# Kernel optimization log

Measured on AMD Instinct MI355X. Metric: run time of the kernel, lower is better.

The kernel has to match this reference:

```python
import jax, jax.numpy as jnp
import numpy as np

B, T, N, M, P = 1024, 128, 128, 256, 256


def _lstm_step(x, h, c, Wih, Whh, bih, bhh):
    # PyTorch LSTM cell: gates ordered i, f, g, o
    g = x @ Wih.T + bih + h @ Whh.T + bhh
    i, f, gg, o = jnp.split(g, 4, axis=-1)
    c_new = jax.nn.sigmoid(f) * c + jax.nn.sigmoid(i) * jnp.tanh(gg)
    h_new = jax.nn.sigmoid(o) * jnp.tanh(c_new)
    return h_new, c_new


def darnn_forward(enc_data, dec_data, enc_Wih, enc_Whh, enc_bih, enc_bhh,
                  We, Ue, ve, Wd, Ud, vd, wt_w, wt_b,
                  dec_Wih, dec_Whh, dec_bih, dec_bhh, l1_w, l1_b, l2_w, l2_b):
    Bsz, Tlen, n = enc_data.shape
    m = enc_Whh.shape[1]
    p = dec_Whh.shape[1]
    # ---- Encoder with input attention ----
    # U_e(data.permute(0,2,1)): (B, n, T); constant across time steps
    Ue_data = jnp.einsum('btn,st->bns', enc_data, Ue)
    def enc_step(carry, x_t):
        h, c = carry                                   # (B, m) each
        q = jnp.concatenate([h, c], axis=-1)           # (B, 2m)
        wq = q @ We.T                                  # (B, T)
        score = jnp.tanh(wq[:, None, :] + Ue_data) @ ve  # (B, n)
        alpha = jax.nn.softmax(score, axis=-1)
        h, c = _lstm_step(alpha * x_t, h, c, enc_Wih, enc_Whh, enc_bih, enc_bhh)
        return (h, c), h
    h0 = jnp.zeros((Bsz, m), enc_data.dtype)
    (_, _), Hs = jax.lax.scan(enc_step, (h0, h0), jnp.swapaxes(enc_data, 0, 1))
    H = jnp.swapaxes(Hs, 0, 1)                         # (B, T, m)
    # ---- Decoder with temporal attention ----
    UH = jnp.einsum('btm,um->btu', H, Ud)              # (B, T, m); constant
    def attn_ctx(d, s):
        q = jnp.concatenate([d, s], axis=-1)           # (B, 2p)
        wq = q @ Wd.T                                  # (B, m)
        score = jnp.tanh(wq[:, None, :] + UH) @ vd     # (B, T)
        beta = jax.nn.softmax(score, axis=-1)
        return jnp.einsum('bt,btm->bm', beta, H)       # (B, m)
    def dec_step(carry, y):
        d, s = carry
        ctx = attn_ctx(d, s)
        y_tilde = jnp.concatenate([y, ctx], axis=-1) @ wt_w.T + wt_b  # (B, 1)
        d, s = _lstm_step(y_tilde, d, s, dec_Wih, dec_Whh, dec_bih, dec_bhh)
        return (d, s), None
    d0 = jnp.zeros((Bsz, p), enc_data.dtype)
    ys = jnp.swapaxes(dec_data[:, :Tlen - 1, :], 0, 1)  # (T-1, B, 1)
    (d, s), _ = jax.lax.scan(dec_step, (d0, d0), ys)
    ctx = attn_ctx(d, s)
    out = jnp.concatenate([d, ctx], axis=-1)            # (B, p + m)
    out = jax.nn.relu(out @ l1_w.T + l1_b) @ l2_w.T + l2_b
    return out.reshape(-1)


def setup_inputs() -> dict:
    key = jax.random.key(0)
    ks = jax.random.split(key, 22)
    f = lambda k, shape: jax.random.normal(k, shape, jnp.float32) * 0.05
    return {
        'enc_data': jax.random.normal(ks[0], (B, T, N), jnp.float32),
        'dec_data': jax.random.normal(ks[1], (B, T, 1), jnp.float32),
        'enc_Wih': f(ks[2], (4 * M, N)), 'enc_Whh': f(ks[3], (4 * M, M)),
        'enc_bih': f(ks[4], (4 * M,)), 'enc_bhh': f(ks[5], (4 * M,)),
        'We': f(ks[6], (T, 2 * M)), 'Ue': f(ks[7], (T, T)), 've': f(ks[8], (T,)),
        'Wd': f(ks[9], (M, 2 * P)), 'Ud': f(ks[10], (M, M)), 'vd': f(ks[11], (M,)),
        'wt_w': f(ks[12], (1, M + 1)), 'wt_b': f(ks[13], (1,)),
        'dec_Wih': f(ks[14], (4 * P, 1)), 'dec_Whh': f(ks[15], (4 * P, P)),
        'dec_bih': f(ks[16], (4 * P,)), 'dec_bhh': f(ks[17], (4 * P,)),
        'l1_w': f(ks[18], (P, M + P)), 'l1_b': f(ks[19], (P,)),
        'l2_w': f(ks[20], (1, P)), 'l2_b': f(ks[21], (1,)),
    }


def reference(enc_data, dec_data, enc_Wih, enc_Whh, enc_bih, enc_bhh,
              We, Ue, ve, Wd, Ud, vd, wt_w, wt_b,
              dec_Wih, dec_Whh, dec_bih, dec_bhh, l1_w, l1_b, l2_w, l2_b):
    return darnn_forward(enc_data, dec_data, enc_Wih, enc_Whh, enc_bih, enc_bhh,
                         We, Ue, ve, Wd, Ud, vd, wt_w, wt_b,
                         dec_Wih, dec_Whh, dec_bih, dec_bhh, l1_w, l1_b, l2_w, l2_b)
```

## Files before the change

kernel.cpp:

```cpp
#include <hip/hip_runtime.h>

typedef unsigned short ushort_t;
typedef unsigned char u8_t;
typedef unsigned int u32_t;
typedef float f32x2 __attribute__((ext_vector_type(2)));

static constexpr int BATCH = 1024;
static constexpr int TT = 128;
static constexpr int NN = 128;
static constexpr int MM = 256;

__device__ __forceinline__ float bf2f(ushort_t u) {
    union { unsigned int i; float f; } v;
    v.i = ((unsigned int)u) << 16;
    return v.f;
}
__device__ __forceinline__ ushort_t f2bf(float f) {
    union { unsigned int i; float f; } v;
    v.f = f;
    unsigned int i = v.i;
    return (ushort_t)((i + 0x7FFFu + ((i >> 16) & 1u)) >> 16);
}
__device__ __forceinline__ u32_t pk2bf(float lo, float hi) {
    return (u32_t)f2bf(lo) | ((u32_t)f2bf(hi) << 16);
}
__device__ __forceinline__ float dot2bf(u32_t a, u32_t b, float c) {
    float d;
    asm("v_dot2_f32_bf16 %0, %1, %2, %3" : "=v"(d) : "v"(a), "v"(b), "v"(c));
    return d;
}
__device__ __forceinline__ void unp8(const int4 w, float* o) {
    union { unsigned int i; float f; } v;
    v.i = ((unsigned int)w.x) << 16;        o[0] = v.f;
    v.i = ((unsigned int)w.x) & 0xffff0000u; o[1] = v.f;
    v.i = ((unsigned int)w.y) << 16;        o[2] = v.f;
    v.i = ((unsigned int)w.y) & 0xffff0000u; o[3] = v.f;
    v.i = ((unsigned int)w.z) << 16;        o[4] = v.f;
    v.i = ((unsigned int)w.z) & 0xffff0000u; o[5] = v.f;
    v.i = ((unsigned int)w.w) << 16;        o[6] = v.f;
    v.i = ((unsigned int)w.w) & 0xffff0000u; o[7] = v.f;
}
__device__ __forceinline__ void unp4(const int2 w, float* o) {
    union { unsigned int i; float f; } v;
    v.i = ((unsigned int)w.x) << 16;        o[0] = v.f;
    v.i = ((unsigned int)w.x) & 0xffff0000u; o[1] = v.f;
    v.i = ((unsigned int)w.y) << 16;        o[2] = v.f;
    v.i = ((unsigned int)w.y) & 0xffff0000u; o[3] = v.f;
}
__device__ __forceinline__ void unp8f8(const int2 w, float* o) {
    f32x2 a = __builtin_amdgcn_cvt_pk_f32_fp8(w.x, false);
    f32x2 b = __builtin_amdgcn_cvt_pk_f32_fp8(w.x, true);
    f32x2 c = __builtin_amdgcn_cvt_pk_f32_fp8(w.y, false);
    f32x2 d = __builtin_amdgcn_cvt_pk_f32_fp8(w.y, true);
    o[0] = a.x; o[1] = a.y; o[2] = b.x; o[3] = b.y;
    o[4] = c.x; o[5] = c.y; o[6] = d.x; o[7] = d.y;
}
__device__ __forceinline__ float tanh_fast(float x) {
    float e = __expf(2.0f * x);
    return 1.0f - __fdividef(2.0f, e + 1.0f);
}
__device__ __forceinline__ float sig_fast(float x) {
    return __fdividef(1.0f, 1.0f + __expf(-x));
}

template<bool WBF16, bool TRANSW, int CMODE, bool RELU>
__global__ __launch_bounds__(256) void gemm_k(
    const float* __restrict__ A1, int lda1, long sA1z, int K1,
    const float* __restrict__ A2, int lda2, int K2,
    const void* __restrict__ W1v, int ldw1, long sW1z,
    const void* __restrict__ W2v, int ldw2,
    const float* __restrict__ bias1,
    void* __restrict__ Cv, int ldc, long sCz)
{
    __shared__ float As[32][68];
    __shared__ float Ws[32][68];
    const int tid = threadIdx.x;
    const int z = blockIdx.z;
    const int m0 = blockIdx.y * 64;
    const int g0 = blockIdx.x * 64;
    const int tm = tid & 15, tn = tid >> 4;
    float acc[4][4];
#pragma unroll
    for (int i = 0; i < 4; ++i)
#pragma unroll
        for (int j = 0; j < 4; ++j) acc[i][j] = 0.0f;

    for (int phase = 0; phase < 2; ++phase) {
        const float* A = (phase == 0) ? (A1 + (long)z * sA1z) : A2;
        const int lda = (phase == 0) ? lda1 : lda2;
        const int K = (phase == 0) ? K1 : K2;
        const int ldw = (phase == 0) ? ldw1 : ldw2;
        const void* Wv = (phase == 0) ? W1v : W2v;
        const long woff = (phase == 0) ? (long)z * sW1z : 0;
        if (A == nullptr || Wv == nullptr || K <= 0) continue;

        for (int k0 = 0; k0 < K; k0 += 32) {
            const int rem = K - k0;
            {
                const int tr0 = tid >> 3;
                const int tk = (tid & 7) * 4;
#pragma unroll
                for (int pass = 0; pass < 2; ++pass) {
                    const int m = tr0 + pass * 32;
                    const float* p = A + (long)(m0 + m) * lda + k0 + tk;
#pragma unroll
                    for (int j = 0; j < 4; ++j) {
                        float v = 0.0f;
                        if (tk + j < rem) v = p[j];
                        As[tk + j][m] = v;
                    }
                }
            }
            if constexpr (TRANSW) {
                const float* W = (const float*)Wv + woff;
                const int gq = (tid & 15) * 4;
                const int kr = tid >> 4;
#pragma unroll
                for (int pass = 0; pass < 2; ++pass) {
                    const int k = kr + pass * 16;
                    const float* p = W + (long)(k0 + k) * ldw + g0 + gq;
                    const bool ok = (k < rem);
#pragma unroll
                    for (int j = 0; j < 4; ++j) {
                        float v = 0.0f;
                        if (ok) v = p[j];
                        Ws[k][gq + j] = v;
                    }
                }
            } else if constexpr (WBF16) {
                const ushort_t* W = (const ushort_t*)Wv + woff;
                const int g = tid >> 2;
                const int tk = (tid & 3) * 8;
                const ushort_t* p = W + (long)(g0 + g) * ldw + k0 + tk;
#pragma unroll
                for (int j = 0; j < 8; ++j) {
                    float v = 0.0f;
                    if (tk + j < rem) v = bf2f(p[j]);
                    Ws[tk + j][g] = v;
                }
            } else {
                const float* W = (const float*)Wv + woff;
                const int tr0 = tid >> 3;
                const int tk = (tid & 7) * 4;
#pragma unroll
                for (int pass = 0; pass < 2; ++pass) {
                    const int g = tr0 + pass * 32;
                    const float* p = W + (long)(g0 + g) * ldw + k0 + tk;
#pragma unroll
                    for (int j = 0; j < 4; ++j) {
                        float v = 0.0f;
                        if (tk + j < rem) v = p[j];
                        Ws[tk + j][g] = v;
                    }
                }
            }
            __syncthreads();
#pragma unroll
            for (int kk = 0; kk < 32; ++kk) {
                const float4 av = *(const float4*)&As[kk][tm * 4];
                const float4 bv = *(const float4*)&Ws[kk][tn * 4];
                const float a[4] = {av.x, av.y, av.z, av.w};
                const float b[4] = {bv.x, bv.y, bv.z, bv.w};
#pragma unroll
                for (int i = 0; i < 4; ++i)
#pragma unroll
                    for (int j = 0; j < 4; ++j)
                        acc[i][j] = fmaf(a[i], b[j], acc[i][j]);
            }
            __syncthreads();
        }
    }
#pragma unroll
    for (int i = 0; i < 4; ++i) {
        const long m = m0 + tm * 4 + i;
        if constexpr (CMODE == 2) {
            float v[4];
#pragma unroll
            for (int j = 0; j < 4; ++j) {
                v[j] = acc[i][j];
                if (bias1) v[j] += bias1[g0 + tn * 4 + j];
                if (RELU) v[j] = fmaxf(v[j], 0.0f);
            }
            int pk = __builtin_amdgcn_cvt_pk_fp8_f32(v[0], v[1], 0, false);
            pk = __builtin_amdgcn_cvt_pk_fp8_f32(v[2], v[3], pk, true);
            *(unsigned int*)((u8_t*)Cv + (long)z * sCz + m * ldc + g0 + tn * 4) =
                (unsigned int)pk;
        } else {
#pragma unroll
            for (int j = 0; j < 4; ++j) {
                const int g = g0 + tn * 4 + j;
                float v = acc[i][j];
                if (bias1) v += bias1[g];
                if (RELU) v = fmaxf(v, 0.0f);
                if constexpr (CMODE == 1)
                    ((ushort_t*)Cv)[(long)z * sCz + m * ldc + g] = f2bf(v);
                else
                    ((float*)Cv)[(long)z * sCz + m * ldc + g] = v;
            }
        }
    }
}

__global__ void prep_encw_k(const float* __restrict__ Wih, const float* __restrict__ Whh,
                            ushort_t* __restrict__ dst) {
    int i = blockIdx.x * 256 + threadIdx.x;
    if (i >= 384 * 1024) return;
    int k = i >> 10, col = i & 1023, u = col >> 2, q = col & 3, g = q * 256 + u;
    float v = (k < 128) ? Wih[g * 128 + k] : Whh[g * 256 + (k - 128)];
    dst[(k >> 1) * 2048 + u * 8 + q * 2 + (k & 1)] = f2bf(v);
}

__global__ void prep_decw_k(const float* __restrict__ Wih, const float* __restrict__ Whh,
                            ushort_t* __restrict__ dst) {
    int i = blockIdx.x * 256 + threadIdx.x;
    if (i >= 257 * 1024) return;
    int k = i >> 10, col = i & 1023, u = col >> 2, q = col & 3, g = q * 256 + u;
    float v = (k == 0) ? Wih[g] : Whh[g * 256 + (k - 1)];
    ushort_t b = f2bf(v);
    if (k == 0) {
        dst[col] = b;
    } else {
        int kk = k - 1;
        dst[1024 + (kk >> 1) * 2048 + u * 8 + q * 2 + (kk & 1)] = b;
    }
}

__global__ void transpose_k(const float* __restrict__ src, float* __restrict__ dst,
                            int R, int C) {
    int i = blockIdx.x * 256 + threadIdx.x;
    if (i < R * C) { int r = i / C, c = i - r * C; dst[c * R + r] = src[i]; }
}

__global__ void packT_k(const float* __restrict__ src, ushort_t* __restrict__ dst,
                        int R, int C) {
    int i = blockIdx.x * 256 + threadIdx.x;
    if (i >= R * C) return;
    int s = i / C, k = i - s * C;
    dst[(k >> 1) * (2 * R) + (s >> 2) * 8 + (s & 3) * 2 + (k & 1)] = f2bf(src[i]);
}

__global__ __launch_bounds__(512) void enc_persist(
    const float* __restrict__ enc_data,
    const u8_t* __restrict__ D,
    const ushort_t* __restrict__ WeB,
    const float* __restrict__ ve,
    const ushort_t* __restrict__ WencB,
    const float* __restrict__ bih, const float* __restrict__ bhh,
    ushort_t* __restrict__ Hbf)
{
    const int tid = threadIdx.x;
    const int b0 = blockIdx.x * 4;
    __shared__ __align__(16) float cs[256][4];
    __shared__ __align__(16) u32_t qpk[256][4];
    __shared__ __align__(16) u32_t xtp[64][4];
    __shared__ __align__(16) float wqp[16][128][4];
    __shared__ __align__(16) float wqs[128][4];
    __shared__ __align__(16) float scp[8][4][128];
    __shared__ float gp[4][4][256];
    __shared__ float ves[128];

    if (tid < 128) ves[tid] = ve[tid];
    if (tid < 256) {
        const float4 z = make_float4(0.f, 0.f, 0.f, 0.f);
        *(float4*)cs[tid] = z;
    }
    {
        uint4 z4 = {0u, 0u, 0u, 0u};
        for (int i = tid; i < 256; i += 512) *(uint4*)qpk[i] = z4;
    }
    const int u = tid & 255;
    const int ks = tid >> 8;
    const float b_i = bih[u] + bhh[u];
    const float b_f = bih[256 + u] + bhh[256 + u];
    const float b_g = bih[512 + u] + bhh[512 + u];
    const float b_o = bih[768 + u] + bhh[768 + u];
    __syncthreads();

    const int kgq = tid >> 5, sv = tid & 31;
    const ushort_t* wq_w = WeB + (long)(kgq * 16) * 256 + sv * 8;
    const int nv = tid & 15, srow = (tid >> 4) & 3, ssl = tid >> 6;
    const u8_t* Dp0 = D + (long)(b0 + srow) * 16384 + (ssl * 16) * 128 + nv * 8;
    const ushort_t* gw = WencB + u * 8;

    float SVe = 0.0f;
#pragma unroll
    for (int s = 0; s < 16; ++s) SVe += ves[ssl * 16 + s];

    for (int t = 0; t < 128; ++t) {
        {
            float a[4][4];
#pragma unroll
            for (int m = 0; m < 4; ++m)
#pragma unroll
                for (int r = 0; r < 4; ++r) a[m][r] = 0.0f;
#pragma unroll 4
            for (int k2 = 0; k2 < 16; ++k2) {
                const uint4 wv = *(const uint4*)(wq_w + k2 * 256);
                const uint4 qv = *(const uint4*)qpk[kgq * 16 + k2];
                const u32_t wa[4] = {wv.x, wv.y, wv.z, wv.w};
                const u32_t qa[4] = {qv.x, qv.y, qv.z, qv.w};
#pragma unroll
                for (int m = 0; m < 4; ++m)
#pragma unroll
                    for (int r = 0; r < 4; ++r)
                        a[m][r] = dot2bf(wa[m], qa[r], a[m][r]);
            }
#pragma unroll
            for (int m = 0; m < 4; ++m)
                *(float4*)wqp[kgq][sv * 4 + m] = make_float4(a[m][0], a[m][1], a[m][2], a[m][3]);
        }
        __syncthreads();
        if (tid < 128) {
            float4 s = *(const float4*)wqp[0][tid];
#pragma unroll
            for (int g = 1; g < 16; ++g) {
                const float4 p = *(const float4*)wqp[g][tid];
                s.x += p.x; s.y += p.y; s.z += p.z; s.w += p.w;
            }
            *(float4*)wqs[tid] = s;
        }
        __syncthreads();
        {
            float a[8];
#pragma unroll
            for (int j = 0; j < 8; ++j) a[j] = 0.0f;
#pragma unroll 4
            for (int s = 0; s < 16; ++s) {
                const int sg = ssl * 16 + s;
                const float w2 = wqs[sg][srow] * 2.0f;
                const float vv = ves[sg];
                const int2 wv2 = *(const int2*)(Dp0 + s * 128);
                float d[8];
                unp8f8(wv2, d);
#pragma unroll
                for (int j = 0; j < 8; ++j) {
                    const float ex = __expf(fmaf(d[j], 2.0f, w2));
                    a[j] = fmaf(vv, __fdividef(1.0f, ex + 1.0f), a[j]);
                }
            }
            *(float4*)&scp[ssl][srow][nv * 8] =
                make_float4(fmaf(-2.f, a[0], SVe), fmaf(-2.f, a[1], SVe),
                            fmaf(-2.f, a[2], SVe), fmaf(-2.f, a[3], SVe));
            *(float4*)&scp[ssl][srow][nv * 8 + 4] =
                make_float4(fmaf(-2.f, a[4], SVe), fmaf(-2.f, a[5], SVe),
                            fmaf(-2.f, a[6], SVe), fmaf(-2.f, a[7], SVe));
        }
        __syncthreads();
        if (tid < 256) {
            const int w = tid >> 6, lane = tid & 63;
            float s0 = 0.0f, s1 = 0.0f;
#pragma unroll
            for (int g = 0; g < 8; ++g) {
                s0 += scp[g][w][lane];
                s1 += scp[g][w][lane + 64];
            }
            float mx = fmaxf(s0, s1);
            for (int o = 32; o > 0; o >>= 1) mx = fmaxf(mx, __shfl_xor(mx, o, 64));
            const float e0 = __expf(s0 - mx), e1 = __expf(s1 - mx);
            float sm = e0 + e1;
            for (int o = 32; o > 0; o >>= 1) sm += __shfl_xor(sm, o, 64);
            const float inv = __fdividef(1.0f, sm);
            const float* xp = enc_data + ((long)(b0 + w) * 128 + t) * 128;
            const float v0 = e0 * inv * xp[lane];
            const float v1 = e1 * inv * xp[lane + 64];
            const float p0 = __shfl_xor(v0, 1, 64);
            const float p1 = __shfl_xor(v1, 1, 64);
            if ((lane & 1) == 0) {
                xtp[lane >> 1][w] = pk2bf(v0, p0);
                xtp[32 + (lane >> 1)][w] = pk2bf(v1, p1);
            }
        }
        __syncthreads();
        float acc[4][4];
#pragma unroll
        for (int q = 0; q < 4; ++q)
#pragma unroll
            for (int r = 0; r < 4; ++r) acc[q][r] = 0.0f;
        if (ks == 0) {
#pragma unroll 4
            for (int p = 0; p < 64; ++p) {
                const uint4 wv = *(const uint4*)(gw + (long)p * 2048);
                const uint4 xv = *(const uint4*)xtp[p];
                const u32_t wa[4] = {wv.x, wv.y, wv.z, wv.w};
                const u32_t xa[4] = {xv.x, xv.y, xv.z, xv.w};
#pragma unroll
                for (int q = 0; q < 4; ++q)
#pragma unroll
                    for (int r = 0; r < 4; ++r)
                        acc[q][r] = dot2bf(wa[q], xa[r], acc[q][r]);
            }
#pragma unroll 4
            for (int p = 64; p < 96; ++p) {
                const uint4 wv = *(const uint4*)(gw + (long)p * 2048);
                const uint4 xv = *(const uint4*)qpk[p - 64];
                const u32_t wa[4] = {wv.x, wv.y, wv.z, wv.w};
                const u32_t xa[4] = {xv.x, xv.y, xv.z, xv.w};
#pragma unroll
                for (int q = 0; q < 4; ++q)
#pragma unroll
                    for (int r = 0; r < 4; ++r)
                        acc[q][r] = dot2bf(wa[q], xa[r], acc[q][r]);
            }
        } else {
#pragma unroll 4
            for (int p = 96; p < 192; ++p) {
                const uint4 wv = *(const uint4*)(gw + (long)p * 2048);
                const uint4 xv = *(const uint4*)qpk[p - 64];
                const u32_t wa[4] = {wv.x, wv.y, wv.z, wv.w};
                const u32_t xa[4] = {xv.x, xv.y, xv.z, xv.w};
#pragma unroll
                for (int q = 0; q < 4; ++q)
#pragma unroll
                    for (int r = 0; r < 4; ++r)
                        acc[q][r] = dot2bf(wa[q], xa[r], acc[q][r]);
            }
#pragma unroll
            for (int q = 0; q < 4; ++q)
#pragma unroll
                for (int r = 0; r < 4; ++r) gp[q][r][u] = acc[q][r];
        }
        __syncthreads();
        if (ks == 0) {
#pragma unroll
            for (int r = 0; r < 4; ++r) {
                const float iv = sig_fast(acc[0][r] + gp[0][r][u] + b_i);
                const float fv = sig_fast(acc[1][r] + gp[1][r][u] + b_f);
                const float gv = tanh_fast(acc[2][r] + gp[2][r][u] + b_g);
                const float ov = sig_fast(acc[3][r] + gp[3][r][u] + b_o);
                const float cn = fv * cs[u][r] + iv * gv;
                const float hn = ov * tanh_fast(cn);
                cs[u][r] = cn;
                const float hp = __shfl_xor(hn, 1, 64);
                const float cp = __shfl_xor(cn, 1, 64);
                if ((u & 1) == 0) {
                    qpk[u >> 1][r] = pk2bf(hn, hp);
                    qpk[128 + (u >> 1)][r] = pk2bf(cn, cp);
                }
                Hbf[((long)(b0 + r) * 128 + t) * 256 + u] = f2bf(hn);
            }
        }
        __syncthreads();
    }
}

__global__ __launch_bounds__(512) void dec_persist(
    const float* __restrict__ dec_data,
    const u8_t* __restrict__ UH2,
    const ushort_t* __restrict__ Hb,
    const ushort_t* __restrict__ WdB,
    const float* __restrict__ vd,
    const ushort_t* __restrict__ WdecB,
    const float* __restrict__ bih, const float* __restrict__ bhh,
    const float* __restrict__ wt_w, const float* __restrict__ wt_b,
    const float* __restrict__ l1T,
    const float* __restrict__ l1_b,
    const float* __restrict__ l2_w, const float* __restrict__ l2_b,
    float* __restrict__ out)
{
    const int tid = threadIdx.x;
    const int b0 = blockIdx.x * 4;
    __shared__ __align__(16) float ds4[256][4];
    __shared__ __align__(16) float ss4[256][4];
    __shared__ __align__(16) u32_t qpk[256][4];
    __shared__ __align__(16) float wqp[8][256][4];
    __shared__ __align__(16) float wqs[256][4];
    __shared__ __align__(16) float scp[8][4][128];
    __shared__ __align__(16) float beta[128][4];
    __shared__ __align__(16) float ctxp[4][4][256];
    __shared__ __align__(16) float ctx4[256][4];
    __shared__ float gp[4][4][256];
    __shared__ __align__(16) float o14[256][4];
    __shared__ float vds[256];
    __shared__ float wt1s[256];
    __shared__ float l2s[256];
    __shared__ __align__(16) float yts[4];

    const int u = tid & 255;
    const int ks = tid >> 8;
    if (tid < 256) {
        vds[tid] = vd[tid];
        wt1s[tid] = wt_w[1 + tid];
        l2s[tid] = l2_w[tid];
        const float4 z = make_float4(0.f, 0.f, 0.f, 0.f);
        *(float4*)ds4[tid] = z;
        *(float4*)ss4[tid] = z;
    }
    {
        uint4 z4 = {0u, 0u, 0u, 0u};
        for (int i = tid; i < 256; i += 512) *(uint4*)qpk[i] = z4;
    }
    const float b_i = bih[u] + bhh[u];
    const float b_f = bih[256 + u] + bhh[256 + u];
    const float b_g = bih[512 + u] + bhh[512 + u];
    const float b_o = bih[768 + u] + bhh[768 + u];
    __syncthreads();

    const int kgq = tid >> 6, mv = tid & 63;
    const ushort_t* wq_w = WdB + (long)(kgq * 32) * 512 + mv * 8;
    const int tv = tid & 15, srow = (tid >> 4) & 3, usl = tid >> 6;
    const u8_t* up0 = UH2 + ((long)(b0 + srow) * 256 + usl * 32) * 128 + tv * 8;
    const int mv8 = tid & 31, crow = (tid >> 5) & 3, ssl2 = tid >> 7;
    const ushort_t* hp0 = Hb + ((long)(b0 + crow) * 128 + ssl2 * 32) * 256 + mv8 * 8;
    const ushort_t* gwp = WdecB + 1024 + u * 8;

    float SVd = 0.0f;
#pragma unroll
    for (int s = 0; s < 32; ++s) SVd += vds[usl * 32 + s];

    for (int td = 0; td < 128; ++td) {
        {
            float a[4][4];
#pragma unroll
            for (int m = 0; m < 4; ++m)
#pragma unroll
                for (int r = 0; r < 4; ++r) a[m][r] = 0.0f;
#pragma unroll 4
            for (int k2 = 0; k2 < 32; ++k2) {
                const uint4 wv = *(const uint4*)(wq_w + k2 * 512);
                const uint4 qv = *(const uint4*)qpk[kgq * 32 + k2];
                const u32_t wa[4] = {wv.x, wv.y, wv.z, wv.w};
                const u32_t qa[4] = {qv.x, qv.y, qv.z, qv.w};
#pragma unroll
                for (int m = 0; m < 4; ++m)
#pragma unroll
                    for (int r = 0; r < 4; ++r)
                        a[m][r] = dot2bf(wa[m], qa[r], a[m][r]);
            }
#pragma unroll
            for (int m = 0; m < 4; ++m)
                *(float4*)wqp[kgq][mv * 4 + m] = make_float4(a[m][0], a[m][1], a[m][2], a[m][3]);
        }
        __syncthreads();
        if (tid < 256) {
            float4 s = *(const float4*)wqp[0][tid];
#pragma unroll
            for (int g = 1; g < 8; ++g) {
                const float4 p = *(const float4*)wqp[g][tid];
                s.x += p.x; s.y += p.y; s.z += p.z; s.w += p.w;
            }
            *(float4*)wqs[tid] = s;
        }
        __syncthreads();
        {
            float a[8];
#pragma unroll
            for (int j = 0; j < 8; ++j) a[j] = 0.0f;
#pragma unroll 4
            for (int uu = 0; uu < 32; ++uu) {
                const int ug = usl * 32 + uu;
                const float w2 = wqs[ug][srow] * 2.0f;
                const float vv = vds[ug];
                const int2 wv2 = *(const int2*)(up0 + uu * 128);
                float d[8];
                unp8f8(wv2, d);
#pragma unroll
                for (int j = 0; j < 8; ++j) {
                    const float ex = __expf(fmaf(d[j], 2.0f, w2));
                    a[j] = fmaf(vv, __fdividef(1.0f, ex + 1.0f), a[j]);
                }
            }
            *(float4*)&scp[usl][srow][tv * 8] =
                make_float4(fmaf(-2.f, a[0], SVd), fmaf(-2.f, a[1], SVd),
                            fmaf(-2.f, a[2], SVd), fmaf(-2.f, a[3], SVd));
            *(float4*)&scp[usl][srow][tv * 8 + 4] =
                make_float4(fmaf(-2.f, a[4], SVd), fmaf(-2.f, a[5], SVd),
                            fmaf(-2.f, a[6], SVd), fmaf(-2.f, a[7], SVd));
        }
        __syncthreads();
        if (tid < 256) {
            const int w = tid >> 6, lane = tid & 63;
            float s0 = 0.0f, s1 = 0.0f;
#pragma unroll
            for (int g = 0; g < 8; ++g) {
                s0 += scp[g][w][lane];
                s1 += scp[g][w][lane + 64];
            }
            float mx = fmaxf(s0, s1);
            for (int o = 32; o > 0; o >>= 1) mx = fmaxf(mx, __shfl_xor(mx, o, 64));
            const float e0 = __expf(s0 - mx), e1 = __expf(s1 - mx);
            float sm = e0 + e1;
            for (int o = 32; o > 0; o >>= 1) sm += __shfl_xor(sm, o, 64);
            const float inv = __fdividef(1.0f, sm);
            beta[lane][w] = e0 * inv;
            beta[lane + 64][w] = e1 * inv;
        }
        __syncthreads();
        {
            float c[8];
#pragma unroll
            for (int j = 0; j < 8; ++j) c[j] = 0.0f;
#pragma unroll 4
            for (int s = 0; s < 32; ++s) {
                const float bt = beta[ssl2 * 32 + s][crow];
                const int4 wv2 = *(const int4*)(hp0 + s * 256);
                float hv[8];
                unp8(wv2, hv);
#pragma unroll
                for (int j = 0; j < 8; ++j)
                    c[j] = fmaf(bt, hv[j], c[j]);
            }
            *(float4*)&ctxp[ssl2][crow][mv8 * 8]     = make_float4(c[0], c[1], c[2], c[3]);
            *(float4*)&ctxp[ssl2][crow][mv8 * 8 + 4] = make_float4(c[4], c[5], c[6], c[7]);
        }
        __syncthreads();
        if (tid < 256) {
            const int m = tid;
            float cr[4];
#pragma unroll
            for (int r = 0; r < 4; ++r)
                cr[r] = ctxp[0][r][m] + ctxp[1][r][m] + ctxp[2][r][m] + ctxp[3][r][m];
            *(float4*)ctx4[m] = make_float4(cr[0], cr[1], cr[2], cr[3]);
        }
        __syncthreads();
        if (td == 127) break;
        if (tid < 256) {
            const int w = tid >> 6, lane = tid & 63;
            float s = ctx4[lane][w] * wt1s[lane]
                    + ctx4[lane + 64][w] * wt1s[lane + 64]
                    + ctx4[lane + 128][w] * wt1s[lane + 128]
                    + ctx4[lane + 192][w] * wt1s[lane + 192];
            for (int o = 32; o > 0; o >>= 1) s += __shfl_xor(s, o, 64);
            if (lane == 0)
                yts[w] = s + wt_b[0] + wt_w[0] * dec_data[(long)(b0 + w) * 128 + td];
        }
        __syncthreads();
        float acc[4][4];
        if (ks == 0) {
            const int2 yv = *(const int2*)(WdecB + u * 4);
            float wy[4]; unp4(yv, wy);
            const float4 y4 = *(const float4*)yts;
            const float ya[4] = {y4.x, y4.y, y4.z, y4.w};
#pragma unroll
            for (int q = 0; q < 4; ++q)
#pragma unroll
                for (int r = 0; r < 4; ++r) acc[q][r] = wy[q] * ya[r];
#pragma unroll 4
            for (int p = 0; p < 64; ++p) {
                const uint4 wv = *(const uint4*)(gwp + (long)p * 2048);
                const uint4 xv = *(const uint4*)qpk[p];
                const u32_t wa[4] = {wv.x, wv.y, wv.z, wv.w};
                const u32_t xa[4] = {xv.x, xv.y, xv.z, xv.w};
#pragma unroll
                for (int q = 0; q < 4; ++q)
#pragma unroll
                    for (int r = 0; r < 4; ++r)
                        acc[q][r] = dot2bf(wa[q], xa[r], acc[q][r]);
            }
        } else {
#pragma unroll
            for (int q = 0; q < 4; ++q)
#pragma unroll
                for (int r = 0; r < 4; ++r) acc[q][r] = 0.0f;
#pragma unroll 4
            for (int p = 64; p < 128; ++p) {
                const uint4 wv = *(const uint4*)(gwp + (long)p * 2048);
                const uint4 xv = *(const uint4*)qpk[p];
                const u32_t wa[4] = {wv.x, wv.y, wv.z, wv.w};
                const u32_t xa[4] = {xv.x, xv.y, xv.z, xv.w};
#pragma unroll
                for (int q = 0; q < 4; ++q)
#pragma unroll
                    for (int r = 0; r < 4; ++r)
                        acc[q][r] = dot2bf(wa[q], xa[r], acc[q][r]);
            }
#pragma unroll
            for (int q = 0; q < 4; ++q)
#pragma unroll
                for (int r = 0; r < 4; ++r) gp[q][r][u] = acc[q][r];
        }
        __syncthreads();
        if (ks == 0) {
#pragma unroll
            for (int r = 0; r < 4; ++r) {
                const float iv = sig_fast(acc[0][r] + gp[0][r][u] + b_i);
                const float fv = sig_fast(acc[1][r] + gp[1][r][u] + b_f);
                const float gv = tanh_fast(acc[2][r] + gp[2][r][u] + b_g);
                const float ov = sig_fast(acc[3][r] + gp[3][r][u] + b_o);
                const float sn = fv * ss4[u][r] + iv * gv;
                const float dn = ov * tanh_fast(sn);
                ss4[u][r] = sn;
                ds4[u][r] = dn;
                const float dp = __shfl_xor(dn, 1, 64);
                const float sp = __shfl_xor(sn, 1, 64);
                if ((u & 1) == 0) {
                    qpk[u >> 1][r] = pk2bf(dn, dp);
                    qpk[128 + (u >> 1)][r] = pk2bf(sn, sp);
                }
            }
        }
        __syncthreads();
    }
    {
        const float* src = l1T + ks * 256 * 256;
        float a0 = 0, a1 = 0, a2 = 0, a3 = 0;
#pragma unroll 4
        for (int k = 0; k < 256; ++k) {
            const float w = src[k * 256 + u];
            const float4 q = (ks == 0) ? *(const float4*)ds4[k]
                                       : *(const float4*)ctx4[k];
            a0 = fmaf(q.x, w, a0); a1 = fmaf(q.y, w, a1);
            a2 = fmaf(q.z, w, a2); a3 = fmaf(q.w, w, a3);
        }
        if (ks == 1) {
            gp[0][0][u] = a0; gp[0][1][u] = a1; gp[0][2][u] = a2; gp[0][3][u] = a3;
        } else {
            gp[1][0][u] = a0; gp[1][1][u] = a1; gp[1][2][u] = a2; gp[1][3][u] = a3;
        }
    }
    __syncthreads();
    if (tid < 256) {
        const float bb = l1_b[tid];
        *(float4*)o14[tid] = make_float4(
            fmaxf(gp[0][0][tid] + gp[1][0][tid] + bb, 0.f),
            fmaxf(gp[0][1][tid] + gp[1][1][tid] + bb, 0.f),
            fmaxf(gp[0][2][tid] + gp[1][2][tid] + bb, 0.f),
            fmaxf(gp[0][3][tid] + gp[1][3][tid] + bb, 0.f));
    }
    __syncthreads();
    if (tid < 256) {
        const int w = tid >> 6, lane = tid & 63;
        float s = o14[lane][w] * l2s[lane]
                + o14[lane + 64][w] * l2s[lane + 64]
                + o14[lane + 128][w] * l2s[lane + 128]
                + o14[lane + 192][w] * l2s[lane + 192];
        for (int o = 32; o > 0; o >>= 1) s += __shfl_xor(s, o, 64);
        if (lane == 0) out[b0 + w] = s + l2_b[0];
    }
}

extern "C" void kernel_launch(void* const* d_in, const int* in_sizes, int n_in,
                              void* d_out, int out_size, void* d_ws, size_t ws_size,
                              hipStream_t stream)
{
    const float* enc_data = (const float*)d_in[0];
    const float* dec_data = (const float*)d_in[1];
    const float* enc_Wih  = (const float*)d_in[2];
    const float* enc_Whh  = (const float*)d_in[3];
    const float* enc_bih  = (const float*)d_in[4];
    const float* enc_bhh  = (const float*)d_in[5];
    const float* We   = (const float*)d_in[6];
    const float* Ue   = (const float*)d_in[7];
    const float* ve   = (const float*)d_in[8];
    const float* Wd   = (const float*)d_in[9];
    const float* Ud   = (const float*)d_in[10];
    const float* vd   = (const float*)d_in[11];
    const float* wt_w = (const float*)d_in[12];
    const float* wt_b = (const float*)d_in[13];
    const float* dec_Wih = (const float*)d_in[14];
    const float* dec_Whh = (const float*)d_in[15];
    const float* dec_bih = (const float*)d_in[16];
    const float* dec_bhh = (const float*)d_in[17];
    const float* l1_w = (const float*)d_in[18];
    const float* l1_b = (const float*)d_in[19];
    const float* l2_w = (const float*)d_in[20];
    const float* l2_b = (const float*)d_in[21];

    ushort_t* Hbf  = (ushort_t*)d_ws;
    u8_t* Dbf      = (u8_t*)(Hbf + (long)BATCH * TT * MM);
    u8_t* UHbf     = Dbf + (long)BATCH * TT * NN;
    ushort_t* WencB = (ushort_t*)(UHbf + (long)BATCH * MM * TT);
    ushort_t* WdecB = WencB + 384 * 1024;
    ushort_t* WeB   = WdecB + 257 * 1024;
    ushort_t* WdB   = WeB + 512 * 128;
    float* l1T      = (float*)(WdB + 512 * 256);

    prep_encw_k<<<1536, 256, 0, stream>>>(enc_Wih, enc_Whh, WencB);
    prep_decw_k<<<1028, 256, 0, stream>>>(dec_Wih, dec_Whh, WdecB);
    packT_k<<<(128 * 512 + 255) / 256, 256, 0, stream>>>(We, WeB, 128, 512);
    packT_k<<<(256 * 512 + 255) / 256, 256, 0, stream>>>(Wd, WdB, 256, 512);
    transpose_k<<<(256 * 512 + 255) / 256, 256, 0, stream>>>(l1_w, l1T, 256, 512);

    gemm_k<false, true, 2, false><<<dim3(NN / 64, TT / 64, BATCH), 256, 0, stream>>>(
        Ue, TT, 0, TT,
        nullptr, 0, 0,
        enc_data, NN, (long)TT * NN,
        nullptr, 0,
        nullptr,
        Dbf, NN, (long)TT * NN);

    enc_persist<<<256, 512, 0, stream>>>(enc_data, Dbf, WeB, ve, WencB,
                                         enc_bih, enc_bhh, Hbf);

    gemm_k<true, false, 2, false><<<dim3(TT / 64, MM / 64, BATCH), 256, 0, stream>>>(
        Ud, MM, 0, MM,
        nullptr, 0, 0,
        Hbf, MM, (long)TT * MM,
        nullptr, 0,
        nullptr,
        UHbf, TT, (long)MM * TT);

    dec_persist<<<256, 512, 0, stream>>>(dec_data, UHbf, Hbf, WdB, vd, WdecB,
                                         dec_bih, dec_bhh, wt_w, wt_b,
                                         l1T, l1_b, l2_w, l2_b, (float*)d_out);
}
```

Before: 9.415 ms.

## Hoist decoder recurrent matmul earlier, pair sigmoid divides, bf16 beta context dot

Moves the decoder LSTM h/s recurrent gate matmul (which depends only on the previous state) up to run alongside the attention query matmul. This removes one barrier and the serial gate phase after the attention and context stages. The tanh-via-exp attention score loop now shares one reciprocal across two elements, with a clamp added to avoid overflow. The context sum packs beta into bf16 pairs and uses v_dot2 with v_perm to interleave H rows. Beta now loses precision to bf16, and the gp exchange relies on the existing barriers for correctness.

Result: faster. 8.004 ms (-15.0%).

```diff
diff --git a/kernel.cpp b/kernel.cpp
--- a/kernel.cpp
+++ b/kernel.cpp
@@ -27,6 +27,11 @@
 __device__ __forceinline__ float dot2bf(u32_t a, u32_t b, float c) {
     float d;
     asm("v_dot2_f32_bf16 %0, %1, %2, %3" : "=v"(d) : "v"(a), "v"(b), "v"(c));
+    return d;
+}
+__device__ __forceinline__ u32_t permb(u32_t s0, u32_t s1, u32_t sel) {
+    u32_t d;
+    asm("v_perm_b32 %0, %1, %2, %3" : "=v"(d) : "v"(s0), "v"(s1), "v"(sel));
     return d;
 }
 __device__ __forceinline__ void unp8(const int4 w, float* o) {
@@ -333,9 +338,13 @@
                 float d[8];
                 unp8f8(wv2, d);
 #pragma unroll
-                for (int j = 0; j < 8; ++j) {
-                    const float ex = __expf(fmaf(d[j], 2.0f, w2));
-                    a[j] = fmaf(vv, __fdividef(1.0f, ex + 1.0f), a[j]);
+                for (int j = 0; j < 8; j += 2) {
+                    const float eA = __expf(fminf(fmaf(d[j],     2.0f, w2), 43.0f));
+                    const float eB = __expf(fminf(fmaf(d[j + 1], 2.0f, w2), 43.0f));
+                    const float pA = eA + 1.0f, pB = eB + 1.0f;
+                    const float rr = __fdividef(1.0f, pA * pB);
+                    a[j]     = fmaf(vv, pB * rr, a[j]);
+                    a[j + 1] = fmaf(vv, pA * rr, a[j + 1]);
                 }
             }
             *(float4*)&scp[ssl][srow][nv * 8] =
@@ -465,7 +474,7 @@
     __shared__ __align__(16) float wqp[8][256][4];
     __shared__ __align__(16) float wqs[256][4];
     __shared__ __align__(16) float scp[8][4][128];
-    __shared__ __align__(16) float beta[128][4];
+    __shared__ __align__(16) u32_t betap[64][4];
     __shared__ __align__(16) float ctxp[4][4][256];
     __shared__ __align__(16) float ctx4[256][4];
     __shared__ float gp[4][4][256];
@@ -508,6 +517,7 @@
     for (int s = 0; s < 32; ++s) SVd += vds[usl * 32 + s];
 
     for (int td = 0; td < 128; ++td) {
+        float gacc[4][4];
         {
             float a[4][4];
 #pragma unroll
@@ -529,6 +539,31 @@
 #pragma unroll
             for (int m = 0; m < 4; ++m)
                 *(float4*)wqp[kgq][mv * 4 + m] = make_float4(a[m][0], a[m][1], a[m][2], a[m][3]);
+        }
+        {
+#pragma unroll
+            for (int q = 0; q < 4; ++q)
+#pragma unroll
+                for (int r = 0; r < 4; ++r) gacc[q][r] = 0.0f;
+            const int pbeg = ks * 64, pend = pbeg + 64;
+#pragma unroll 4
+            for (int p = pbeg; p < pend; ++p) {
+                const uint4 wv = *(const uint4*)(gwp + (long)p * 2048);
+                const uint4 xv = *(const uint4*)qpk[p];
+                const u32_t wa[4] = {wv.x, wv.y, wv.z, wv.w};
+                const u32_t xa[4] = {xv.x, xv.y, xv.z, xv.w};
+#pragma unroll
+                for (int q = 0; q < 4; ++q)
+#pragma unroll
+                    for (int r = 0; r < 4; ++r)
+                        gacc[q][r] = dot2bf(wa[q], xa[r], gacc[q][r]);
+            }
+            if (ks != 0) {
+#pragma unroll
+                for (int q = 0; q < 4; ++q)
+#pragma unroll
+                    for (int r = 0; r < 4; ++r) gp[q][r][u] = gacc[q][r];
+            }
         }
         __syncthreads();
         if (tid < 256) {
@@ -554,9 +589,13 @@
                 float d[8];
                 unp8f8(wv2, d);
 #pragma unroll
-                for (int j = 0; j < 8; ++j) {
-                    const float ex = __expf(fmaf(d[j], 2.0f, w2));
-                    a[j] = fmaf(vv, __fdividef(1.0f, ex + 1.0f), a[j]);
+                for (int j = 0; j < 8; j += 2) {
+                    const float eA = __expf(fminf(fmaf(d[j],     2.0f, w2), 43.0f));
+                    const float eB = __expf(fminf(fmaf(d[j + 1], 2.0f, w2), 43.0f));
+                    const float pA = eA + 1.0f, pB = eB + 1.0f;
+                    const float rr = __fdividef(1.0f, pA * pB);
+                    a[j]     = fmaf(vv, pB * rr, a[j]);
+                    a[j + 1] = fmaf(vv, pA * rr, a[j + 1]);
                 }
             }
             *(float4*)&scp[usl][srow][tv * 8] =
@@ -581,8 +620,14 @@
             float sm = e0 + e1;
             for (int o = 32; o > 0; o >>= 1) sm += __shfl_xor(sm, o, 64);
             const float inv = __fdividef(1.0f, sm);
-            beta[lane][w] = e0 * inv;
-            beta[lane + 64][w] = e1 * inv;
+            const float bv0 = e0 * inv;
+            const float bv1 = e1 * inv;
+            const float q0 = __shfl_xor(bv0, 1, 64);
+            const float q1 = __shfl_xor(bv1, 1, 64);
+            if ((lane & 1) == 0) {
+                betap[lane >> 1][w] = pk2bf(bv0, q0);
+                betap[32 + (lane >> 1)][w] = pk2bf(bv1, q1);
+            }
         }
         __syncthreads();
         {
@@ -590,14 +635,19 @@
 #pragma unroll
             for (int j = 0; j < 8; ++j) c[j] = 0.0f;
 #pragma unroll 4
-            for (int s = 0; s < 32; ++s) {
-                const float bt = beta[ssl2 * 32 + s][crow];
-                const int4 wv2 = *(const int4*)(hp0 + s * 256);
-                float hv[8];
-                unp8(wv2, hv);
-#pragma unroll
-                for (int j = 0; j < 8; ++j)
-                    c[j] = fmaf(bt, hv[j], c[j]);
+            for (int sp = 0; sp < 16; ++sp) {
+                const u32_t bt = betap[ssl2 * 16 + sp][crow];
+                const uint4 A = *(const uint4*)(hp0 + (2 * sp) * 256);
+                const uint4 B = *(const uint4*)(hp0 + (2 * sp + 1) * 256);
+                const u32_t Aa[4] = {A.x, A.y, A.z, A.w};
+                const u32_t Ba[4] = {B.x, B.y, B.z, B.w};
+#pragma unroll
+                for (int x = 0; x < 4; ++x) {
+                    const u32_t lo = permb(Aa[x], Ba[x], 0x01000504u);
+                    const u32_t hi = permb(Aa[x], Ba[x], 0x03020706u);
+                    c[2 * x]     = dot2bf(bt, lo, c[2 * x]);
+                    c[2 * x + 1] = dot2bf(bt, hi, c[2 * x + 1]);
+                }
             }
             *(float4*)&ctxp[ssl2][crow][mv8 * 8]     = make_float4(c[0], c[1], c[2], c[3]);
             *(float4*)&ctxp[ssl2][crow][mv8 * 8 + 4] = make_float4(c[4], c[5], c[6], c[7]);
@@ -624,58 +674,17 @@
                 yts[w] = s + wt_b[0] + wt_w[0] * dec_data[(long)(b0 + w) * 128 + td];
         }
         __syncthreads();
-        float acc[4][4];
         if (ks == 0) {
-            const int2 yv = *(const int2*)(WdecB + u * 4);
-            float wy[4]; unp4(yv, wy);
+            float wy[4];
+            unp4(*(const int2*)(WdecB + u * 4), wy);
             const float4 y4 = *(const float4*)yts;
             const float ya[4] = {y4.x, y4.y, y4.z, y4.w};
 #pragma unroll
-            for (int q = 0; q < 4; ++q)
-#pragma unroll
-                for (int r = 0; r < 4; ++r) acc[q][r] = wy[q] * ya[r];
-#pragma unroll 4
-            for (int p = 0; p < 64; ++p) {
-                const uint4 wv = *(const uint4*)(gwp + (long)p * 2048);
-                const uint4 xv = *(const uint4*)qpk[p];
-                const u32_t wa[4] = {wv.x, wv.y, wv.z, wv.w};
-                const u32_t xa[4] = {xv.x, xv.y, xv.z, xv.w};
-#pragma unroll
-                for (int q = 0; q < 4; ++q)
-#pragma unroll
-                    for (int r = 0; r < 4; ++r)
-                        acc[q][r] = dot2bf(wa[q], xa[r], acc[q][r]);
-            }
-        } else {
-#pragma unroll
-            for (int q = 0; q < 4; ++q)
-#pragma unroll
-                for (int r = 0; r < 4; ++r) acc[q][r] = 0.0f;
-#pragma unroll 4
-            for (int p = 64; p < 128; ++p) {
-                const uint4 wv = *(const uint4*)(gwp + (long)p * 2048);
-                const uint4 xv = *(const uint4*)qpk[p];
-                const u32_t wa[4] = {wv.x, wv.y, wv.z, wv.w};
-                const u32_t xa[4] = {xv.x, xv.y, xv.z, xv.w};
-#pragma unroll
-                for (int q = 0; q < 4; ++q)
-#pragma unroll
-                    for (int r = 0; r < 4; ++r)
-                        acc[q][r] = dot2bf(wa[q], xa[r], acc[q][r]);
-            }
-#pragma unroll
-            for (int q = 0; q < 4; ++q)
-#pragma unroll
-                for (int r = 0; r < 4; ++r) gp[q][r][u] = acc[q][r];
-        }
-        __syncthreads();
-        if (ks == 0) {
-#pragma unroll
             for (int r = 0; r < 4; ++r) {
-                const float iv = sig_fast(acc[0][r] + gp[0][r][u] + b_i);
-                const float fv = sig_fast(acc[1][r] + gp[1][r][u] + b_f);
-                const float gv = tanh_fast(acc[2][r] + gp[2][r][u] + b_g);
-                const float ov = sig_fast(acc[3][r] + gp[3][r][u] + b_o);
+                const float iv = sig_fast(gacc[0][r] + gp[0][r][u] + wy[0] * ya[r] + b_i);
+                const float fv = sig_fast(gacc[1][r] + gp[1][r][u] + wy[1] * ya[r] + b_f);
+                const float gv = tanh_fast(gacc[2][r] + gp[2][r][u] + wy[2] * ya[r] + b_g);
+                const float ov = sig_fast(gacc[3][r] + gp[3][r][u] + wy[3] * ya[r] + b_o);
                 const float sn = fv * ss4[u][r] + iv * gv;
                 const float dn = ov * tanh_fast(sn);
                 ss4[u][r] = sn;
```
